# Performance work log

Hardware: AMD Instinct MI355X
Metric: run time of the kernel (lower is better)

## Reference

```python
import jax, jax.numpy as jnp
import numpy as np

N_EMBD = 768
N_HEAD = 12
B, T = 2, 2048


def setup_inputs() -> dict:
    key = jax.random.key(0)
    ks = jax.random.split(key, 8)
    C = N_EMBD
    s = 0.02
    return {
        "x": jax.random.normal(ks[0], (B, T, C), jnp.float32),
        "ln1_g": jnp.ones((C,), jnp.float32),
        "ln1_b": jnp.zeros((C,), jnp.float32),
        "w_attn": jax.random.normal(ks[1], (C, 3 * C), jnp.float32) * s,
        "b_attn": jnp.zeros((3 * C,), jnp.float32),
        "w_attn_proj": jax.random.normal(ks[2], (C, C), jnp.float32) * s,
        "b_attn_proj": jnp.zeros((C,), jnp.float32),
        "ln2_g": jnp.ones((C,), jnp.float32),
        "ln2_b": jnp.zeros((C,), jnp.float32),
        "w_fc": jax.random.normal(ks[3], (C, 4 * C), jnp.float32) * s,
        "b_fc": jnp.zeros((4 * C,), jnp.float32),
        "w_mlp_proj": jax.random.normal(ks[4], (4 * C, C), jnp.float32) * s,
        "b_mlp_proj": jnp.zeros((C,), jnp.float32),
    }


def _layernorm(x, g, b, eps=1e-5):
    mu = jnp.mean(x, axis=-1, keepdims=True)
    var = jnp.mean(jnp.square(x - mu), axis=-1, keepdims=True)
    return (x - mu) * jax.lax.rsqrt(var + eps) * g + b


def _new_gelu(x):
    c = np.sqrt(2.0 / np.pi).astype(np.float32)
    return 0.5 * x * (1.0 + jnp.tanh(c * (x + 0.044715 * x * x * x)))


def _block(x, ln1_g, ln1_b, w_attn, b_attn, w_attn_proj, b_attn_proj,
           ln2_g, ln2_b, w_fc, b_fc, w_mlp_proj, b_mlp_proj):
    Bx, Tx, C = x.shape
    hd = C // N_HEAD
    h = _layernorm(x, ln1_g, ln1_b)
    qkv = h @ w_attn + b_attn  # [B,T,3C]
    q, k, v = jnp.split(qkv, 3, axis=-1)
    # [B,H,T,hd]
    q = q.reshape(Bx, Tx, N_HEAD, hd).transpose(0, 2, 1, 3)
    k = k.reshape(Bx, Tx, N_HEAD, hd).transpose(0, 2, 1, 3)
    v = v.reshape(Bx, Tx, N_HEAD, hd).transpose(0, 2, 1, 3)
    att = jnp.einsum('bhqd,bhkd->bhqk', q, k) * (1.0 / np.sqrt(hd))
    causal = jnp.tril(jnp.ones((Tx, Tx), bool))
    att = jnp.where(causal[None, None], att, -jnp.inf)
    att = jax.nn.softmax(att, axis=-1)
    y = jnp.einsum('bhqk,bhkd->bhqd', att, v)
    y = y.transpose(0, 2, 1, 3).reshape(Bx, Tx, C)
    x = x + y @ w_attn_proj + b_attn_proj
    h2 = _layernorm(x, ln2_g, ln2_b)
    x = x + _new_gelu(h2 @ w_fc + b_fc) @ w_mlp_proj + b_mlp_proj
    return x


def reference(x, ln1_g, ln1_b, w_attn, b_attn, w_attn_proj, b_attn_proj,
              ln2_g, ln2_b, w_fc, b_fc, w_mlp_proj, b_mlp_proj):
    return _block(x, ln1_g, ln1_b, w_attn, b_attn, w_attn_proj, b_attn_proj,
                  ln2_g, ln2_b, w_fc, b_fc, w_mlp_proj, b_mlp_proj)
```

## Files before the change

### kernel.cpp

```cpp
#include <hip/hip_runtime.h>
#include <hip/hip_bf16.h>
#include <math.h>

#define N_EMBD 768
#define N_HEAD 12
#define BATCH  2
#define SEQ    2048
#define ROWS   (BATCH*SEQ)
#define C3     (3*N_EMBD)

typedef __bf16 bf16;
typedef __attribute__((ext_vector_type(8))) __bf16 bf16x8;
typedef __attribute__((ext_vector_type(4))) float f32x4;

__device__ __forceinline__ void async16(const bf16* g, bf16* l) {
    __builtin_amdgcn_global_load_lds(
        (const __attribute__((address_space(1))) uint32_t*)g,
        (__attribute__((address_space(3))) uint32_t*)l, 16, 0, 0);
}

__global__ __launch_bounds__(256) void k_transpose_all(
    const float* __restrict__ w0, bf16* __restrict__ o0,
    const float* __restrict__ w1, bf16* __restrict__ o1,
    const float* __restrict__ w2, bf16* __restrict__ o2,
    const float* __restrict__ w3, bf16* __restrict__ o3)
{
    __shared__ bf16 tile[32][33];
    int bid = blockIdx.x;
    const float* in; bf16* out; int K, N, local;
    if      (bid < 1728) { in = w0; out = o0; K = 768;  N = 2304; local = bid; }
    else if (bid < 2304) { in = w1; out = o1; K = 768;  N = 768;  local = bid - 1728; }
    else if (bid < 4608) { in = w2; out = o2; K = 768;  N = 3072; local = bid - 2304; }
    else                 { in = w3; out = o3; K = 3072; N = 768;  local = bid - 4608; }
    int nt = N / 32;
    int n0 = (local % nt) * 32, k0 = (local / nt) * 32;
    int tc = threadIdx.x & 31, tr = threadIdx.x >> 5;
    #pragma unroll
    for (int i = 0; i < 4; i++) {
        int r = tr + i * 8;
        tile[r][tc] = (bf16)in[(size_t)(k0 + r) * N + n0 + tc];
    }
    __syncthreads();
    #pragma unroll
    for (int i = 0; i < 4; i++) {
        int r = tr + i * 8;
        out[(size_t)(n0 + r) * K + k0 + tc] = tile[tc][r];
    }
}

__global__ __launch_bounds__(256) void k_vtrans(
    const bf16* __restrict__ qkv, bf16* __restrict__ vt)
{
    __shared__ bf16 tile[32][33];
    int tt = blockIdx.x;
    int bh = blockIdx.y;
    int dt = blockIdx.z;
    int b = bh / N_HEAD, h = bh % N_HEAD;
    int tc = threadIdx.x & 31, tr = threadIdx.x >> 5;
    #pragma unroll
    for (int i = 0; i < 4; i++) {
        int r = tr + i * 8;
        tile[r][tc] = qkv[(size_t)(b * SEQ + tt * 32 + r) * C3 + 2 * N_EMBD + h * 64 + dt * 32 + tc];
    }
    __syncthreads();
    #pragma unroll
    for (int i = 0; i < 4; i++) {
        int r = tr + i * 8;
        vt[(size_t)(bh * 64 + dt * 32 + r) * SEQ + tt * 32 + tc] = tile[tc][r];
    }
}

__global__ __launch_bounds__(256) void k_layernorm(
    const float* __restrict__ x, const float* __restrict__ g,
    const float* __restrict__ b, bf16* __restrict__ out)
{
    int wave = threadIdx.x >> 6, lane = threadIdx.x & 63;
    int row = blockIdx.x * 4 + wave;
    const float4* xr = (const float4*)(x + (size_t)row * N_EMBD);
    const float4* g4 = (const float4*)g;
    const float4* b4 = (const float4*)b;
    float4 v[3];
    float s = 0.f, sq = 0.f;
    #pragma unroll
    for (int i = 0; i < 3; i++) {
        v[i] = xr[lane + 64 * i];
        s  += v[i].x + v[i].y + v[i].z + v[i].w;
        sq += v[i].x * v[i].x + v[i].y * v[i].y + v[i].z * v[i].z + v[i].w * v[i].w;
    }
    #pragma unroll
    for (int off = 32; off > 0; off >>= 1) {
        s  += __shfl_xor(s, off);
        sq += __shfl_xor(sq, off);
    }
    float mu  = s * (1.f / N_EMBD);
    float var = sq * (1.f / N_EMBD) - mu * mu;
    float rs  = rsqrtf(var + 1e-5f);
    bf16* orow = out + (size_t)row * N_EMBD;
    #pragma unroll
    for (int i = 0; i < 3; i++) {
        float4 gv = g4[lane + 64 * i], bv = b4[lane + 64 * i];
        union { ushort4 u4; bf16 e[4]; } pk;
        pk.e[0] = (bf16)((v[i].x - mu) * rs * gv.x + bv.x);
        pk.e[1] = (bf16)((v[i].y - mu) * rs * gv.y + bv.y);
        pk.e[2] = (bf16)((v[i].z - mu) * rs * gv.z + bv.z);
        pk.e[3] = (bf16)((v[i].w - mu) * rs * gv.w + bv.w);
        *(ushort4*)&orow[(lane + 64 * i) * 4] = pk.u4;
    }
}

template<int BN, int ACT, bool RES, bool OUT_BF16, bool MSWAP, bool DBUF>
__global__ __launch_bounds__(256) void k_gemm(
    const bf16* __restrict__ A, const bf16* __restrict__ Bt,
    const float* __restrict__ bias, const float* __restrict__ res,
    void* __restrict__ outp, int M, int N, int K)
{
    constexpr int WC  = BN / 64;
    constexpr int WR  = 4 / WC;
    constexpr int RPW = 128 / WR;
    constexpr int MI  = RPW / 16;
    constexpr int NB  = DBUF ? 2 : 1;
    __shared__ __align__(16) bf16 As[NB][128 * 64];
    __shared__ __align__(16) bf16 Bs[NB][BN * 64];
    int n0 = (MSWAP ? blockIdx.y : blockIdx.x) * BN;
    int m0 = (MSWAP ? blockIdx.x : blockIdx.y) * 128;
    int t = threadIdx.x;
    int lane = t & 63, wave = t >> 6;
    int wr = wave / WC, wc = wave % WC;
    int quad = lane >> 4, l16 = lane & 15;

    f32x4 acc[MI][4];
    #pragma unroll
    for (int i = 0; i < MI; i++)
        #pragma unroll
        for (int j = 0; j < 4; j++) acc[i][j] = (f32x4){0.f, 0.f, 0.f, 0.f};

    int sr = t >> 3;
    int sc = t & 7;
    int gsw = (sc ^ (sr & 7)) * 8;

    auto stage = [&](int k0, int bi) {
        #pragma unroll
        for (int p = 0; p < 4; p++) {
            int r = sr + p * 32;
            async16(&A[(size_t)(m0 + r) * K + k0 + gsw], &As[bi][r * 64 + sc * 8]);
        }
        #pragma unroll
        for (int p = 0; p < BN / 32; p++) {
            int r = sr + p * 32;
            async16(&Bt[(size_t)(n0 + r) * K + k0 + gsw], &Bs[bi][r * 64 + sc * 8]);
        }
    };
    auto compute = [&](int bi) {
        #pragma unroll
        for (int kh = 0; kh < 2; kh++) {
            bf16x8 af[MI], bfv[4];
            #pragma unroll
            for (int i = 0; i < MI; i++)
                af[i]  = *(bf16x8*)&As[bi][(wr * RPW + i * 16 + l16) * 64 + (((quad + 4 * kh) ^ (l16 & 7)) * 8)];
            #pragma unroll
            for (int j = 0; j < 4; j++)
                bfv[j] = *(bf16x8*)&Bs[bi][(wc * 64 + j * 16 + l16) * 64 + (((quad + 4 * kh) ^ (l16 & 7)) * 8)];
            #pragma unroll
            for (int i = 0; i < MI; i++)
                #pragma unroll
                for (int j = 0; j < 4; j++)
                    acc[i][j] = __builtin_amdgcn_mfma_f32_16x16x32_bf16(af[i], bfv[j], acc[i][j], 0, 0, 0);
        }
    };

    if (DBUF) {
        stage(0, 0);
        int bi = 0;
        for (int k0 = 0; k0 < K; k0 += 64, bi ^= 1) {
            __syncthreads();
            if (k0 + 64 < K) stage(k0 + 64, bi ^ 1);
            compute(bi);
        }
    } else {
        for (int k0 = 0; k0 < K; k0 += 64) {
            __syncthreads();
            stage(k0, 0);
            __syncthreads();
            compute(0);
        }
    }

    float* outf = (float*)outp;
    bf16*  outb = (bf16*)outp;
    #pragma unroll
    for (int i = 0; i < MI; i++) {
        #pragma unroll
        for (int j = 0; j < 4; j++) {
            int col = n0 + wc * 64 + j * 16 + l16;
            float bv = bias[col];
            #pragma unroll
            for (int r = 0; r < 4; r++) {
                int row = m0 + wr * RPW + i * 16 + quad * 4 + r;
                float v = acc[i][j][r] + bv;
                if (ACT == 1) {
                    float z = 0.7978845608f * (v + 0.044715f * v * v * v);
                    v = v / (1.f + __expf(-2.f * z));
                }
                if (RES) v += res[(size_t)row * N + col];
                if (OUT_BF16) outb[(size_t)row * N + col] = (bf16)v;
                else          outf[(size_t)row * N + col] = v;
            }
        }
    }
}

__global__ __launch_bounds__(256) void k_gemm2(
    const bf16* __restrict__ A, const bf16* __restrict__ Bt,
    const float* __restrict__ bias, const float* __restrict__ res,
    float* __restrict__ outp, int M, int N, int K)
{
    __shared__ __align__(16) bf16 As[2][64 * 64];
    __shared__ __align__(16) bf16 Bs[2][64 * 64];
    int m0 = blockIdx.x * 64, n0 = blockIdx.y * 64;
    int t = threadIdx.x;
    int lane = t & 63, w = t >> 6;
    int wr = w >> 1, wcol = w & 1;
    int quad = lane >> 4, l16 = lane & 15;

    f32x4 acc[2][2];
    #pragma unroll
    for (int i = 0; i < 2; i++)
        #pragma unroll
        for (int j = 0; j < 2; j++) acc[i][j] = (f32x4){0.f, 0.f, 0.f, 0.f};

    int sr = t >> 3;
    int sc = t & 7;
    int gsw = (sc ^ (sr & 7)) * 8;

    auto stage = [&](int k0, int bi) {
        #pragma unroll
        for (int p = 0; p < 2; p++) {
            int r = sr + p * 32;
            async16(&A[(size_t)(m0 + r) * K + k0 + gsw], &As[bi][r * 64 + sc * 8]);
            async16(&Bt[(size_t)(n0 + r) * K + k0 + gsw], &Bs[bi][r * 64 + sc * 8]);
        }
    };
    auto compute = [&](int bi) {
        #pragma unroll
        for (int kh = 0; kh < 2; kh++) {
            int rsw = ((quad + 4 * kh) ^ (l16 & 7)) * 8;
            bf16x8 af[2], bfv[2];
            #pragma unroll
            for (int i = 0; i < 2; i++)
                af[i]  = *(bf16x8*)&As[bi][(wr * 32 + i * 16 + l16) * 64 + rsw];
            #pragma unroll
            for (int j = 0; j < 2; j++)
                bfv[j] = *(bf16x8*)&Bs[bi][(wcol * 32 + j * 16 + l16) * 64 + rsw];
            #pragma unroll
            for (int i = 0; i < 2; i++)
                #pragma unroll
                for (int j = 0; j < 2; j++)
                    acc[i][j] = __builtin_amdgcn_mfma_f32_16x16x32_bf16(af[i], bfv[j], acc[i][j], 0, 0, 0);
        }
    };

    stage(0, 0);
    int bi = 0;
    for (int k0 = 0; k0 < K; k0 += 64, bi ^= 1) {
        __syncthreads();
        if (k0 + 64 < K) stage(k0 + 64, bi ^ 1);
        compute(bi);
    }

    #pragma unroll
    for (int i = 0; i < 2; i++) {
        #pragma unroll
        for (int j = 0; j < 2; j++) {
            int col = n0 + wcol * 32 + j * 16 + l16;
            float bv = bias[col];
            #pragma unroll
            for (int r = 0; r < 4; r++) {
                int row = m0 + wr * 32 + i * 16 + quad * 4 + r;
                outp[(size_t)row * N + col] = acc[i][j][r] + bv + res[(size_t)row * N + col];
            }
        }
    }
}

__global__ __launch_bounds__(256) void k_flash(
    const bf16* __restrict__ qkv, const bf16* __restrict__ vt, bf16* __restrict__ y)
{
    __shared__ __align__(16) bf16 Ks[2][64 * 64];
    __shared__ __align__(16) bf16 VTl[2][64 * 64];
    __shared__ __align__(16) bf16 Ps[4][16 * 64];
    int bid = blockIdx.x;
    int hi = bid >> 8;
    int lo = bid & 255;
    int g  = lo >> 3;
    int e  = lo & 7;
    int bh = hi * 8 + e;
    int qt;
    if      (hi == 0) qt = g;
    else if (hi == 1) qt = (g + 16) & 31;
    else              qt = (g < 16) ? (30 - 2 * g) : (63 - 2 * g);
    int b = bh / N_HEAD, h = bh % N_HEAD;
    int t = threadIdx.x, lane = t & 63, wave = t >> 6;
    int quad = lane >> 4, l16 = lane & 15;
    int qbase = qt * 64 + wave * 16;

    bf16x8 qa[2];
    {
        const bf16* qrow = qkv + (size_t)(b * SEQ + qbase + l16) * C3 + h * 64;
        #pragma unroll
        for (int kh = 0; kh < 2; kh++) {
            union { uint4 u4; bf16 e8[8]; bf16x8 vv; } uq;
            uq.u4 = *(const uint4*)&qrow[quad * 8 + kh * 32];
            #pragma unroll
            for (int j = 0; j < 8; j++) uq.e8[j] = (bf16)((float)uq.e8[j] * 0.125f);
            qa[kh] = uq.vv;
        }
    }
    float l_part[4] = {0.f, 0.f, 0.f, 0.f};
    f32x4 o[4];
    #pragma unroll
    for (int j = 0; j < 4; j++) o[j] = (f32x4){0.f, 0.f, 0.f, 0.f};

    int sr = t >> 3;
    int sc = t & 7;
    int gsw = (sc ^ (sr & 7)) * 8;

    const bf16* kg = qkv + (size_t)b * SEQ * C3 + N_EMBD + h * 64;
    const bf16* vg = vt + (size_t)bh * 64 * SEQ;

    auto stage = [&](int tile, int bufi) {
        int k0 = tile * 64;
        #pragma unroll
        for (int p = 0; p < 2; p++) {
            int rr = sr + 32 * p;
            async16(&kg[(size_t)(k0 + rr) * C3 + gsw],  &Ks[bufi][rr * 64 + sc * 8]);
            async16(&vg[(size_t)rr * SEQ + k0 + gsw], &VTl[bufi][rr * 64 + sc * 8]);
        }
    };

    int ntiles = qt + 1;
    stage(0, 0);

    for (int tt = 0; tt < ntiles; tt++) {
        int bufi = tt & 1;
        int k0 = tt * 64;
        __syncthreads();
        if (tt + 1 < ntiles) stage(tt + 1, bufi ^ 1);

        f32x4 s[4];
        __builtin_amdgcn_s_setprio(1);
        #pragma unroll
        for (int nt = 0; nt < 4; nt++) {
            bf16x8 b0 = *(bf16x8*)&Ks[bufi][(nt * 16 + l16) * 64 + (((quad    ) ^ (l16 & 7)) * 8)];
            bf16x8 b1 = *(bf16x8*)&Ks[bufi][(nt * 16 + l16) * 64 + (((quad + 4) ^ (l16 & 7)) * 8)];
            f32x4 z = (f32x4){0.f, 0.f, 0.f, 0.f};
            z = __builtin_amdgcn_mfma_f32_16x16x32_bf16(qa[0], b0, z, 0, 0, 0);
            z = __builtin_amdgcn_mfma_f32_16x16x32_bf16(qa[1], b1, z, 0, 0, 0);
            s[nt] = z;
        }
        __builtin_amdgcn_s_setprio(0);
        bool diag = (tt == qt);
        float p[4][4];
        #pragma unroll
        for (int nt = 0; nt < 4; nt++) {
            int key = k0 + nt * 16 + l16;
            #pragma unroll
            for (int r = 0; r < 4; r++) {
                float pv = __expf(s[nt][r]);
                if (diag && key > qbase + quad * 4 + r) pv = 0.f;
                p[nt][r] = pv;
                l_part[r] += pv;
            }
        }
        #pragma unroll
        for (int nt = 0; nt < 4; nt++)
            #pragma unroll
            for (int r = 0; r < 4; r++) {
                int q = quad * 4 + r;
                Ps[wave][q * 64 + ((nt * 16 + l16) ^ ((q & 7) << 3))] = (bf16)p[nt][r];
            }
        bf16x8 pa[2];
        #pragma unroll
        for (int kt = 0; kt < 2; kt++)
            pa[kt] = *(bf16x8*)&Ps[wave][l16 * 64 + ((kt * 32 + quad * 8) ^ ((l16 & 7) << 3))];
        __builtin_amdgcn_s_setprio(1);
        #pragma unroll
        for (int jt = 0; jt < 4; jt++) {
            int d = jt * 16 + l16;
            #pragma unroll
            for (int kt = 0; kt < 2; kt++) {
                bf16x8 vb = *(bf16x8*)&VTl[bufi][d * 64 + (((quad + 4 * kt) ^ (l16 & 7)) * 8)];
                o[jt] = __builtin_amdgcn_mfma_f32_16x16x32_bf16(pa[kt], vb, o[jt], 0, 0, 0);
            }
        }
        __builtin_amdgcn_s_setprio(0);
    }
    #pragma unroll
    for (int r = 0; r < 4; r++) {
        #pragma unroll
        for (int off = 8; off > 0; off >>= 1) l_part[r] += __shfl_xor(l_part[r], off);
    }
    #pragma unroll
    for (int jt = 0; jt < 4; jt++)
        #pragma unroll
        for (int r = 0; r < 4; r++) {
            int q = qbase + quad * 4 + r;
            y[(size_t)(b * SEQ + q) * N_EMBD + h * 64 + jt * 16 + l16] =
                (bf16)(o[jt][r] / l_part[r]);
        }
}

extern "C" void kernel_launch(void* const* d_in, const int* in_sizes, int n_in,
                              void* d_out, int out_size, void* d_ws, size_t ws_size,
                              hipStream_t stream) {
    const float* x           = (const float*)d_in[0];
    const float* ln1_g       = (const float*)d_in[1];
    const float* ln1_b       = (const float*)d_in[2];
    const float* w_attn      = (const float*)d_in[3];
    const float* b_attn      = (const float*)d_in[4];
    const float* w_attn_proj = (const float*)d_in[5];
    const float* b_attn_proj = (const float*)d_in[6];
    const float* ln2_g       = (const float*)d_in[7];
    const float* ln2_b       = (const float*)d_in[8];
    const float* w_fc        = (const float*)d_in[9];
    const float* b_fc        = (const float*)d_in[10];
    const float* w_mlp_proj  = (const float*)d_in[11];
    const float* b_mlp_proj  = (const float*)d_in[12];

    char* ws = (char*)d_ws;
    size_t off = 0;
    auto alloc = [&](size_t n) -> void* {
        off = (off + 255) & ~(size_t)255;
        void* p = ws + off;
        off += n;
        return p;
    };
    bf16* wqkvT  = (bf16*)alloc((size_t)C3 * N_EMBD * 2);
    bf16* wprojT = (bf16*)alloc((size_t)N_EMBD * N_EMBD * 2);
    bf16* wfcT   = (bf16*)alloc((size_t)4 * N_EMBD * N_EMBD * 2);
    bf16* wmlpT  = (bf16*)alloc((size_t)N_EMBD * 4 * N_EMBD * 2);
    bf16* hbuf   = (bf16*)alloc((size_t)ROWS * N_EMBD * 2);
    float* x2    = (float*)alloc((size_t)ROWS * N_EMBD * 4);
    bf16* yb     = (bf16*)alloc((size_t)ROWS * N_EMBD * 2);
    bf16* vtb    = (bf16*)alloc((size_t)BATCH * N_HEAD * 64 * SEQ * 2);
    bf16* big    = (bf16*)alloc((size_t)ROWS * 4 * N_EMBD * 2);
    bf16* qkvb   = big;
    bf16* actb   = big;

    k_transpose_all<<<6912, 256, 0, stream>>>(w_attn, wqkvT, w_attn_proj, wprojT,
                                              w_fc, wfcT, w_mlp_proj, wmlpT);

    k_layernorm<<<ROWS / 4, 256, 0, stream>>>(x, ln1_g, ln1_b, hbuf);
    k_gemm<128, 0, false, true,  true,  false><<<dim3(ROWS / 128, C3 / 128), 256, 0, stream>>>(
        hbuf, wqkvT,  b_attn,      nullptr, qkvb, ROWS, C3,     N_EMBD);
    k_vtrans<<<dim3(SEQ / 32, BATCH * N_HEAD, 2), 256, 0, stream>>>(qkvb, vtb);
    k_flash<<<768, 256, 0, stream>>>(qkvb, vtb, yb);
    k_gemm2<<<dim3(ROWS / 64, N_EMBD / 64), 256, 0, stream>>>(
        yb,   wprojT, b_attn_proj, x,       x2,   ROWS, N_EMBD, N_EMBD);
    k_layernorm<<<ROWS / 4, 256, 0, stream>>>(x2, ln2_g, ln2_b, hbuf);
    k_gemm<128, 1, false, true,  true,  false><<<dim3(ROWS / 128, 3072 / 128), 256, 0, stream>>>(
        hbuf, wfcT,   b_fc,        nullptr, actb, ROWS, 3072,   N_EMBD);
    k_gemm2<<<dim3(ROWS / 64, N_EMBD / 64), 256, 0, stream>>>(
        actb, wmlpT,  b_mlp_proj,  x2, (float*)d_out, ROWS, N_EMBD, 3072);
}
```

Measured before the change: 265.9 us.

## Split causal flash attention along keys and add a combine kernel

```diff
diff --git a/kernel.cpp b/kernel.cpp
--- a/kernel.cpp
+++ b/kernel.cpp
@@ -283,21 +283,31 @@
 }
 
 __global__ __launch_bounds__(256) void k_flash(
-    const bf16* __restrict__ qkv, const bf16* __restrict__ vt, bf16* __restrict__ y)
+    const bf16* __restrict__ qkv, const bf16* __restrict__ vt,
+    float* __restrict__ opart, float* __restrict__ lpart)
 {
     __shared__ __align__(16) bf16 Ks[2][64 * 64];
     __shared__ __align__(16) bf16 VTl[2][64 * 64];
     __shared__ __align__(16) bf16 Ps[4][16 * 64];
+
     int bid = blockIdx.x;
-    int hi = bid >> 8;
-    int lo = bid & 255;
-    int g  = lo >> 3;
-    int e  = lo & 7;
-    int bh = hi * 8 + e;
-    int qt;
-    if      (hi == 0) qt = g;
-    else if (hi == 1) qt = (g + 16) & 31;
-    else              qt = (g < 16) ? (30 - 2 * g) : (63 - 2 * g);
+    int qt = 0, piece = 0, bh = 0;
+    {
+        int acc = 0;
+        #pragma unroll 1
+        for (int q = 31; q >= 0; q--) {
+            int nsq = (q + 8) >> 3;
+            int cnt = 24 * nsq;
+            if (bid < acc + cnt) { qt = q; int r = bid - acc; piece = r / 24; bh = r % 24; break; }
+            acc += cnt;
+        }
+    }
+    int ns    = (qt + 8) >> 3;
+    int total = qt + 1;
+    int base  = total / ns, rem = total % ns;
+    int t0 = piece * base + (piece < rem ? piece : rem);
+    int t1 = t0 + base + (piece < rem ? 1 : 0);
+
     int b = bh / N_HEAD, h = bh % N_HEAD;
     int t = threadIdx.x, lane = t & 63, wave = t >> 6;
     int quad = lane >> 4, l16 = lane & 15;
@@ -305,13 +315,14 @@
 
     bf16x8 qa[2];
     {
+        const float qsc = 0.125f * 1.44269504089f;
         const bf16* qrow = qkv + (size_t)(b * SEQ + qbase + l16) * C3 + h * 64;
         #pragma unroll
         for (int kh = 0; kh < 2; kh++) {
             union { uint4 u4; bf16 e8[8]; bf16x8 vv; } uq;
             uq.u4 = *(const uint4*)&qrow[quad * 8 + kh * 32];
             #pragma unroll
-            for (int j = 0; j < 8; j++) uq.e8[j] = (bf16)((float)uq.e8[j] * 0.125f);
+            for (int j = 0; j < 8; j++) uq.e8[j] = (bf16)((float)uq.e8[j] * qsc);
             qa[kh] = uq.vv;
         }
     }
@@ -337,14 +348,13 @@
         }
     };
 
-    int ntiles = qt + 1;
-    stage(0, 0);
-
-    for (int tt = 0; tt < ntiles; tt++) {
-        int bufi = tt & 1;
+    stage(t0, 0);
+
+    for (int tt = t0; tt < t1; tt++) {
+        int bufi = (tt - t0) & 1;
         int k0 = tt * 64;
         __syncthreads();
-        if (tt + 1 < ntiles) stage(tt + 1, bufi ^ 1);
+        if (tt + 1 < t1) stage(tt + 1, bufi ^ 1);
 
         f32x4 s[4];
         __builtin_amdgcn_s_setprio(1);
@@ -365,7 +375,7 @@
             int key = k0 + nt * 16 + l16;
             #pragma unroll
             for (int r = 0; r < 4; r++) {
-                float pv = __expf(s[nt][r]);
+                float pv = exp2f(s[nt][r]);
                 if (diag && key > qbase + quad * 4 + r) pv = 0.f;
                 p[nt][r] = pv;
                 l_part[r] += pv;
@@ -403,10 +413,37 @@
     for (int jt = 0; jt < 4; jt++)
         #pragma unroll
         for (int r = 0; r < 4; r++) {
-            int q = qbase + quad * 4 + r;
-            y[(size_t)(b * SEQ + q) * N_EMBD + h * 64 + jt * 16 + l16] =
-                (bf16)(o[jt][r] / l_part[r]);
-        }
+            size_t row = (size_t)piece * ROWS + b * SEQ + qbase + quad * 4 + r;
+            opart[row * N_EMBD + h * 64 + jt * 16 + l16] = o[jt][r];
+        }
+    if (l16 == 0) {
+        #pragma unroll
+        for (int r = 0; r < 4; r++) {
+            size_t row = (size_t)piece * ROWS + b * SEQ + qbase + quad * 4 + r;
+            lpart[row * N_HEAD + h] = l_part[r];
+        }
+    }
+}
+
+__global__ __launch_bounds__(256) void k_combine(
+    const float* __restrict__ opart, const float* __restrict__ lpart,
+    bf16* __restrict__ y)
+{
+    int row = blockIdx.x;
+    int q = row & (SEQ - 1);
+    int ns = ((q >> 6) + 8) >> 3;
+    int t = threadIdx.x;
+    #pragma unroll
+    for (int i = 0; i < 3; i++) {
+        int col = t + 256 * i;
+        float ov = 0.f, lv = 0.f;
+        for (int p = 0; p < ns; p++) {
+            size_t prow = (size_t)p * ROWS + row;
+            ov += opart[prow * N_EMBD + col];
+            lv += lpart[prow * N_HEAD + (col >> 6)];
+        }
+        y[(size_t)row * N_EMBD + col] = (bf16)(ov / lv);
+    }
 }
 
 extern "C" void kernel_launch(void* const* d_in, const int* in_sizes, int n_in,
@@ -445,6 +482,8 @@
     bf16* big    = (bf16*)alloc((size_t)ROWS * 4 * N_EMBD * 2);
     bf16* qkvb   = big;
     bf16* actb   = big;
+    float* opartb = (float*)alloc((size_t)4 * ROWS * N_EMBD * 4);
+    float* lpartb = (float*)alloc((size_t)4 * ROWS * N_HEAD * 4);
 
     k_transpose_all<<<6912, 256, 0, stream>>>(w_attn, wqkvT, w_attn_proj, wprojT,
                                               w_fc, wfcT, w_mlp_proj, wmlpT);
@@ -453,7 +492,8 @@
     k_gemm<128, 0, false, true,  true,  false><<<dim3(ROWS / 128, C3 / 128), 256, 0, stream>>>(
         hbuf, wqkvT,  b_attn,      nullptr, qkvb, ROWS, C3,     N_EMBD);
     k_vtrans<<<dim3(SEQ / 32, BATCH * N_HEAD, 2), 256, 0, stream>>>(qkvb, vtb);
-    k_flash<<<768, 256, 0, stream>>>(qkvb, vtb, yb);
+    k_flash<<<1920, 256, 0, stream>>>(qkvb, vtb, opartb, lpartb);
+    k_combine<<<ROWS, 256, 0, stream>>>(opartb, lpartb, yb);
     k_gemm2<<<dim3(ROWS / 64, N_EMBD / 64), 256, 0, stream>>>(
         yb,   wprojT, b_attn_proj, x,       x2,   ROWS, N_EMBD, N_EMBD);
     k_layernorm<<<ROWS / 4, 256, 0, stream>>>(x2, ln2_g, ln2_b, hbuf);
```

New measurement: 269.9 us. No clear change (+1.5%).
